# Optimization experiments

Hardware: AMD Instinct MI355X
Metric: run time of the kernel (lower is better)

The kernel has to match this reference:

```python
import jax, jax.numpy as jnp
import numpy as np

B, H, W = 32, 224, 224
K, KS = 64, 7


def setup_inputs() -> dict:
    key = jax.random.key(0)
    k1, k2 = jax.random.split(key)
    x = jax.random.normal(k1, (B, H, W), dtype=jnp.float32)
    # nn.init.normal_(mean=0, std=1/kernel_size**2)
    kernels = jax.random.normal(k2, (K, KS, KS), dtype=jnp.float32) / (KS ** 2)
    return {"x": x, "kernels": kernels}


def reference(x, kernels):
    # x: [B, H, W] single-channel; kernels: [K, ks, ks]
    # Valid cross-correlation (the torch loop does patch * kernel, no flip),
    # stride 1, no padding -> output [B, K, H-ks+1, W-ks+1]
    lhs = x[:, None, :, :]            # [B, 1, H, W]
    rhs = kernels[:, None, :, :]      # [K, 1, ks, ks]
    out = jax.lax.conv_general_dilated(
        lhs, rhs,
        window_strides=(1, 1),
        padding="VALID",
        dimension_numbers=("NCHW", "OIHW", "NCHW"),
    )
    return out
```

## Files before the change

### kernel.cpp

```cpp
#include <hip/hip_runtime.h>

#define BATCH 32
#define HIN 224
#define WIN 224
#define KCH 64
#define KS 7
#define OH 218
#define OW 218

#define TILE_H 32
#define IN_TILE_H 38
#define LDS_STRIDE 240
#define CH_PER_BLOCK 8
#define NBANDS 7
#define OUT_TILE_F (TILE_H * OW)

typedef float f32x4 __attribute__((ext_vector_type(4)));

__global__ __launch_bounds__(256, 2)
void conv7x7_kernel(const float* __restrict__ x,
                    const float* __restrict__ kern,
                    float* __restrict__ out) {
    __shared__ float tile[IN_TILE_H][LDS_STRIDE];
    __shared__ float otile[OUT_TILE_F];

    const int band = blockIdx.x;
    const int kg   = blockIdx.y;
    const int b    = blockIdx.z;

    const int h0 = band * TILE_H;

    const int tid  = threadIdx.x;
    const int wv   = tid >> 6;
    const int lane = tid & 63;

    if (tid < IN_TILE_H) {
        f32x4 z = {0.f, 0.f, 0.f, 0.f};
        *reinterpret_cast<f32x4*>(&tile[tid][0]) = z;
    }

    const float* xb = x + b * (HIN * WIN);
    const int NV = (LDS_STRIDE - 4) / 4;
    for (int idx = tid; idx < IN_TILE_H * NV; idx += 256) {
        const int r  = idx / NV;
        const int cg = idx - r * NV;
        const int sr = h0 + r;
        const int sc = cg * 4;
        float4 v;
        if (sr < HIN && sc + 3 < WIN) {
            v = *reinterpret_cast<const float4*>(xb + sr * WIN + sc);
        } else {
            float t0 = (sr < HIN && sc + 0 < WIN) ? xb[sr * WIN + sc + 0] : 0.f;
            float t1 = (sr < HIN && sc + 1 < WIN) ? xb[sr * WIN + sc + 1] : 0.f;
            float t2 = (sr < HIN && sc + 2 < WIN) ? xb[sr * WIN + sc + 2] : 0.f;
            float t3 = (sr < HIN && sc + 3 < WIN) ? xb[sr * WIN + sc + 3] : 0.f;
            v = make_float4(t0, t1, t2, t3);
        }
        *reinterpret_cast<float4*>(&tile[r][4 + sc]) = v;
    }
    __syncthreads();

    const int r0 = wv * 8;
    const int cl = (lane < 54) ? lane : 54;
    const int c0 = cl * 4;

    #pragma unroll 1
    for (int kk = 0; kk < CH_PER_BLOCK; ++kk) {
        const int k = kg * CH_PER_BLOCK + kk;
        const float* __restrict__ wk = kern + k * (KS * KS);

        #pragma unroll
        for (int i = 0; i < 8; ++i) {
            const int base = (i & 1) ? c0 : c0 + 4;
            const int sh   = (i & 1) ? 2 : 0;

            f32x4 acc = {0.f, 0.f, 0.f, 0.f};

            #pragma unroll
            for (int ki = 0; ki < 7; ++ki) {
                const float* rp = &tile[r0 + i + ki][0];
                const f32x4 w0 = *reinterpret_cast<const f32x4*>(rp + base);
                const f32x4 w1 = *reinterpret_cast<const f32x4*>(rp + base + 4);
                const f32x4 w2 = *reinterpret_cast<const f32x4*>(rp + base + 8);

                #pragma unroll
                for (int kj = 0; kj < 7; ++kj) {
                    const float wgt = wk[ki * 7 + kj];
                    #pragma unroll
                    for (int j = 0; j < 4; ++j) {
                        const int n = sh + kj + j;
                        const float xv = (n < 4) ? w0[n]
                                       : (n < 8) ? w1[n - 4]
                                                 : w2[n - 8];
                        acc[j] = fmaf(wgt, xv, acc[j]);
                    }
                }
            }

            const int ot = (r0 + i) * OW;
            if ((i & 1) == 0) {
                if (lane < 54) {
                    *reinterpret_cast<f32x4*>(&otile[ot + c0]) = acc;
                } else if (lane == 54) {
                    otile[ot + 216] = acc[0];
                    otile[ot + 217] = acc[1];
                }
            } else {
                if (lane == 0) {
                    otile[ot]     = acc[2];
                    otile[ot + 1] = acc[3];
                } else if (lane <= 54) {
                    *reinterpret_cast<f32x4*>(&otile[ot + c0 - 2]) = acc;
                }
            }
        }
        __syncthreads();

        const size_t A0 = (size_t)(b * KCH + k) * (OH * OW) + (size_t)h0 * OW;
        const int   m   = (int)(A0 & 15);
        float* gbase = out + A0;
        const int Lr = ((h0 + TILE_H <= OH) ? TILE_H : (OH - h0)) * OW;

        #pragma unroll 1
        for (int g = tid * 4 - m; g < Lr; g += 1024) {
            if (g >= 0 && g + 4 <= Lr) {
                *reinterpret_cast<f32x4*>(gbase + g) =
                    *reinterpret_cast<const f32x4*>(&otile[g]);
            } else {
                #pragma unroll
                for (int u = 0; u < 4; ++u) {
                    const int gu = g + u;
                    if (gu >= 0 && gu < Lr) gbase[gu] = otile[gu];
                }
            }
        }
        __syncthreads();
    }
}

extern "C" void kernel_launch(void* const* d_in, const int* in_sizes, int n_in,
                              void* d_out, int out_size, void* d_ws, size_t ws_size,
                              hipStream_t stream) {
    const float* x    = (const float*)d_in[0];
    const float* kern = (const float*)d_in[1];
    float* out        = (float*)d_out;

    dim3 grid(NBANDS, KCH / CH_PER_BLOCK, BATCH);
    dim3 block(256, 1, 1);
    conv7x7_kernel<<<grid, block, 0, stream>>>(x, kern, out);
}
```

Measured before the change: 580.6 us.

## Reuse each LDS input row across all eight output rows per thread

Reorders the per-channel loops so each thread walks the 14 input rows once, loading a 16-float window per row and accumulating into all eight output-row accumulators that use it. This replaces the earlier scheme that reloaded the 7 input rows separately for every output row, cutting LDS reads roughly fourfold. In exchange the thread holds eight vec4 accumulators plus a wider window, which raises register pressure under the 2-blocks launch bound and could cause spills.

```diff
diff --git a/kernel.cpp b/kernel.cpp
--- a/kernel.cpp
+++ b/kernel.cpp
@@ -69,48 +69,59 @@
         const int k = kg * CH_PER_BLOCK + kk;
         const float* __restrict__ wk = kern + k * (KS * KS);
 
+        f32x4 acc[8];
         #pragma unroll
         for (int i = 0; i < 8; ++i) {
-            const int base = (i & 1) ? c0 : c0 + 4;
-            const int sh   = (i & 1) ? 2 : 0;
+            f32x4 z = {0.f, 0.f, 0.f, 0.f};
+            acc[i] = z;
+        }
 
-            f32x4 acc = {0.f, 0.f, 0.f, 0.f};
+        #pragma unroll
+        for (int ii = 0; ii < 14; ++ii) {
+            const float* rp = &tile[r0 + ii][0];
+            const f32x4 w0 = *reinterpret_cast<const f32x4*>(rp + c0);
+            const f32x4 w1 = *reinterpret_cast<const f32x4*>(rp + c0 + 4);
+            const f32x4 w2 = *reinterpret_cast<const f32x4*>(rp + c0 + 8);
+            const f32x4 w3 = *reinterpret_cast<const f32x4*>(rp + c0 + 12);
 
             #pragma unroll
-            for (int ki = 0; ki < 7; ++ki) {
-                const float* rp = &tile[r0 + i + ki][0];
-                const f32x4 w0 = *reinterpret_cast<const f32x4*>(rp + base);
-                const f32x4 w1 = *reinterpret_cast<const f32x4*>(rp + base + 4);
-                const f32x4 w2 = *reinterpret_cast<const f32x4*>(rp + base + 8);
-
-                #pragma unroll
-                for (int kj = 0; kj < 7; ++kj) {
-                    const float wgt = wk[ki * 7 + kj];
+            for (int i = 0; i < 8; ++i) {
+                const int ki = ii - i;
+                if (ki >= 0 && ki < 7) {
+                    const int sh = (i & 1) ? 2 : 4;
                     #pragma unroll
-                    for (int j = 0; j < 4; ++j) {
-                        const int n = sh + kj + j;
-                        const float xv = (n < 4) ? w0[n]
-                                       : (n < 8) ? w1[n - 4]
-                                                 : w2[n - 8];
-                        acc[j] = fmaf(wgt, xv, acc[j]);
+                    for (int kj = 0; kj < 7; ++kj) {
+                        const float wgt = wk[ki * 7 + kj];
+                        #pragma unroll
+                        for (int j = 0; j < 4; ++j) {
+                            const int n = sh + kj + j;
+                            const float xv = (n < 4)  ? w0[n]
+                                           : (n < 8)  ? w1[n - 4]
+                                           : (n < 12) ? w2[n - 8]
+                                                      : w3[n - 12];
+                            acc[i][j] = fmaf(wgt, xv, acc[i][j]);
+                        }
                     }
                 }
             }
+        }
 
+        #pragma unroll
+        for (int i = 0; i < 8; ++i) {
             const int ot = (r0 + i) * OW;
             if ((i & 1) == 0) {
                 if (lane < 54) {
-                    *reinterpret_cast<f32x4*>(&otile[ot + c0]) = acc;
+                    *reinterpret_cast<f32x4*>(&otile[ot + c0]) = acc[i];
                 } else if (lane == 54) {
-                    otile[ot + 216] = acc[0];
-                    otile[ot + 217] = acc[1];
+                    otile[ot + 216] = acc[i][0];
+                    otile[ot + 217] = acc[i][1];
                 }
             } else {
                 if (lane == 0) {
-                    otile[ot]     = acc[2];
-                    otile[ot + 1] = acc[3];
+                    otile[ot]     = acc[i][2];
+                    otile[ot + 1] = acc[i][3];
                 } else if (lane <= 54) {
-                    *reinterpret_cast<f32x4*>(&otile[ot + c0 - 2]) = acc;
+                    *reinterpret_cast<f32x4*>(&otile[ot + c0 - 2]) = acc[i];
                 }
             }
         }
```

Measured after the change: 542.8 us. -6.5%, faster.
